# Optimization experiments

Hardware: AMD Instinct MI355X
Metric: run time of the kernel (lower is better)

The kernel has to match this reference:

```python
import jax, jax.numpy as jnp
import numpy as np

N_NODES = 100000
N_EDGES = 1600000
G_DIM, H1_DIM, H2_DIM = 128, 64, 64
N_REL = 8          # 2 * n_speakers**2, n_speakers=2
N_BASES = 30


def setup_inputs() -> dict:
    key = jax.random.key(0)
    ks = jax.random.split(key, 12)
    sc = lambda *s: 1.0 / np.sqrt(s[0])
    return {
        "node_features": jax.random.normal(ks[0], (N_NODES, G_DIM), jnp.float32),
        "edge_index": jax.random.randint(ks[1], (2, N_EDGES), 0, N_NODES),
        "edge_norm": jax.random.uniform(ks[2], (N_EDGES,), jnp.float32),
        "edge_type": jax.random.randint(ks[3], (N_EDGES,), 0, N_REL),
        # RGCNConv params (basis decomposition)
        "basis": jax.random.normal(ks[4], (N_BASES, G_DIM, H1_DIM), jnp.float32) * sc(G_DIM),
        "comp": jax.random.normal(ks[5], (N_REL, N_BASES), jnp.float32) * sc(N_BASES),
        "root": jax.random.normal(ks[6], (G_DIM, H1_DIM), jnp.float32) * sc(G_DIM),
        "bias1": jnp.zeros((H1_DIM,), jnp.float32),
        # GraphConv params
        "w_rel": jax.random.normal(ks[7], (H1_DIM, H2_DIM), jnp.float32) * sc(H1_DIM),
        "b_rel": jnp.zeros((H2_DIM,), jnp.float32),
        "w_root": jax.random.normal(ks[8], (H1_DIM, H2_DIM), jnp.float32) * sc(H1_DIM),
    }


def reference(node_features, edge_index, edge_norm, edge_type,
              basis, comp, root, bias1, w_rel, b_rel, w_root):
    N = node_features.shape[0]
    src, dst = edge_index[0], edge_index[1]

    # ---- RGCNConv: per-relation mean aggregation, basis-decomposed weights ----
    W = jnp.einsum('rb,bio->rio', comp, basis)          # [R, g, h1]
    x_src = node_features[src]                           # [E, g] gather
    out1 = node_features @ root + bias1                  # root + bias
    for r in range(N_REL):                               # fixed small relation set
        m = (edge_type == r).astype(node_features.dtype)  # [E]
        s = jax.ops.segment_sum(x_src * m[:, None], dst, num_segments=N)  # [N, g]
        cnt = jax.ops.segment_sum(m, dst, num_segments=N)                 # [N]
        h = s / jnp.maximum(cnt, 1.0)[:, None]            # mean aggr (0 if no edges)
        out1 = out1 + h @ W[r]

    # ---- GraphConv: sum of x_j * edge_weight -> lin_rel, plus lin_root ----
    agg = jax.ops.segment_sum(out1[src] * edge_norm[:, None], dst, num_segments=N)
    out2 = agg @ w_rel + b_rel + out1 @ w_root
    return out2
```

## Files before the change

### kernel.cpp

```cpp
#include <hip/hip_runtime.h>
#include <hip/hip_bf16.h>

#define NN 100000
#define NE 1600000
#define GD 128
#define H1 64
#define H2 64
#define NREL 8
#define NBASES 30
#define NBTOT 576

#define NPB 256
#define NBUCK ((NN + NPB - 1) / NPB)
#define NWGA 128
#define ECHUNK ((NE + NWGA - 1) / NWGA)

typedef __attribute__((ext_vector_type(8))) short bf16x8;
typedef __attribute__((ext_vector_type(4))) float f32x4;

static __device__ __forceinline__ unsigned short f2bf(float x) {
    __hip_bfloat16 h = __float2bfloat16(x);
    return *reinterpret_cast<unsigned short*>(&h);
}
static __device__ __forceinline__ float bf2f(unsigned short u) {
    return __uint_as_float(((unsigned)u) << 16);
}
static __device__ __forceinline__ float bflo(unsigned u) {
    return __uint_as_float(u << 16);
}
static __device__ __forceinline__ float bfhi(unsigned u) {
    return __uint_as_float(u & 0xffff0000u);
}

__global__ void prep_kernel(const float* __restrict__ basis,
                            const float* __restrict__ comp,
                            const float* __restrict__ root,
                            const float* __restrict__ w_rel,
                            const float* __restrict__ w_root,
                            unsigned short* __restrict__ WcatT,
                            unsigned short* __restrict__ B2T)
{
    int idx = blockIdx.x * blockDim.x + threadIdx.x;
    const int totalW = NBTOT * GD;
    if (idx < totalW) {
        int c = idx / GD;
        int i = idx % GD;
        float v;
        if (c < NREL * H1) {
            int r = c >> 6, o = c & 63;
            float acc = 0.f;
            #pragma unroll 5
            for (int b = 0; b < NBASES; ++b)
                acc += comp[r * NBASES + b] * basis[(b * GD + i) * H1 + o];
            v = acc;
        } else {
            v = root[i * H1 + (c - NREL * H1)];
        }
        WcatT[idx] = f2bf(v);
    } else {
        int j = idx - totalW;
        if (j < H2 * GD) {
            int o = j / GD, i = j % GD;
            float v = (i < H1) ? w_rel[i * H2 + o] : w_root[(i - H1) * H2 + o];
            B2T[j] = f2bf(v);
        }
    }
}

__global__ __launch_bounds__(512)
void bucket_count(const int* __restrict__ ei, unsigned* __restrict__ bcnt)
{
    __shared__ unsigned l[NBUCK];
    int t = threadIdx.x;
    int c0 = blockIdx.x * ECHUNK;
    int c1 = c0 + ECHUNK; if (c1 > NE) c1 = NE;
    for (int i = t; i < NBUCK; i += 512) l[i] = 0;
    __syncthreads();
    for (int e = c0 + t; e < c1; e += 512)
        atomicAdd(&l[ei[NE + e] >> 8], 1u);
    __syncthreads();
    for (int i = t; i < NBUCK; i += 512)
        if (l[i]) atomicAdd(&bcnt[i], l[i]);
}

__global__ __launch_bounds__(512)
void bucket_scan(const unsigned* __restrict__ bcnt,
                 unsigned* __restrict__ boff,
                 unsigned* __restrict__ bcur,
                 unsigned* __restrict__ off)
{
    __shared__ unsigned s[512];
    int t = threadIdx.x;
    unsigned v = (t < NBUCK) ? bcnt[t] : 0u;
    s[t] = v;
    __syncthreads();
    for (int st = 1; st < 512; st <<= 1) {
        unsigned u = (t >= st) ? s[t - st] : 0u;
        __syncthreads();
        s[t] += u;
        __syncthreads();
    }
    if (t < NBUCK) { boff[t] = s[t] - v; bcur[t] = s[t] - v; }
    if (t == 511) { boff[NBUCK] = s[511]; off[NN] = s[511]; }
}

__global__ __launch_bounds__(512)
void partition_a(const int* __restrict__ ei, const int* __restrict__ et,
                 const float* __restrict__ enorm,
                 unsigned* __restrict__ bcur,
                 uint2* __restrict__ tmp)
{
    __shared__ unsigned lcnt[NBUCK], wbase[NBUCK], lcur[NBUCK];
    int t = threadIdx.x;
    int c0 = blockIdx.x * ECHUNK;
    int c1 = c0 + ECHUNK; if (c1 > NE) c1 = NE;
    for (int i = t; i < NBUCK; i += 512) { lcnt[i] = 0; lcur[i] = 0; }
    __syncthreads();
    for (int e = c0 + t; e < c1; e += 512) {
        int dst = ei[NE + e];
        atomicAdd(&lcnt[dst >> 8], 1u);
    }
    __syncthreads();
    for (int i = t; i < NBUCK; i += 512)
        wbase[i] = atomicAdd(&bcur[i], lcnt[i]);
    __syncthreads();
    for (int e = c0 + t; e < c1; e += 512) {
        int src = ei[e], dst = ei[NE + e], r = et[e];
        int b = dst >> 8;
        unsigned pos = wbase[b] + atomicAdd(&lcur[b], 1u);
        unsigned dl = (unsigned)(dst & (NPB - 1));
        tmp[pos] = make_uint2((dl << 24) | ((unsigned)src << 3) | (unsigned)r,
                              __float_as_uint(enorm[e]));
    }
}

__global__ __launch_bounds__(512)
void partition_b(const unsigned* __restrict__ boff,
                 const uint2* __restrict__ tmp,
                 uint2* __restrict__ csr,
                 unsigned* __restrict__ off,
                 unsigned* __restrict__ cnt)
{
    __shared__ unsigned lcnt[NPB * NREL];
    __shared__ unsigned sscan[256];
    __shared__ unsigned lcur[NPB];
    int b = blockIdx.x, t = threadIdx.x;
    int nlo = b * NPB;
    int nn = NN - nlo; if (nn > NPB) nn = NPB;
    for (int i = t; i < NPB * NREL; i += 512) lcnt[i] = 0;
    __syncthreads();
    unsigned bstart = boff[b], bend = boff[b + 1];
    for (unsigned j = bstart + t; j < bend; j += 512) {
        unsigned x = tmp[j].x;
        atomicAdd(&lcnt[((x >> 24) << 3) | (x & 7u)], 1u);
    }
    __syncthreads();
    unsigned tot = 0;
    if (t < 256) {
        if (t < nn) {
            #pragma unroll
            for (int r = 0; r < NREL; ++r) tot += lcnt[t * NREL + r];
        }
        sscan[t] = tot;
    }
    __syncthreads();
    for (int st = 1; st < 256; st <<= 1) {
        unsigned u = (t < 256 && t >= st) ? sscan[t - st] : 0u;
        __syncthreads();
        if (t < 256) sscan[t] += u;
        __syncthreads();
    }
    if (t < nn) {
        unsigned ex = bstart + sscan[t] - tot;
        off[nlo + t] = ex;
        lcur[t] = ex;
        *reinterpret_cast<uint4*>(&cnt[(size_t)(nlo + t) * NREL]) =
            *reinterpret_cast<uint4*>(&lcnt[t * NREL]);
        *reinterpret_cast<uint4*>(&cnt[(size_t)(nlo + t) * NREL + 4]) =
            *reinterpret_cast<uint4*>(&lcnt[t * NREL + 4]);
    }
    __syncthreads();
    for (unsigned j = bstart + t; j < bend; j += 512) {
        uint2 rec = tmp[j];
        unsigned dl = rec.x >> 24;
        unsigned p = atomicAdd(&lcur[dl], 1u);
        csr[p] = make_uint2(rec.x & 0x00FFFFFFu, rec.y);
    }
}

template<int MODE>
__global__ __launch_bounds__(256)
void mfma_gemm(const void* __restrict__ Avoid,
               const unsigned short* __restrict__ Bt,
               int M,
               const float* __restrict__ bias,
               unsigned short* __restrict__ y,
               unsigned short* __restrict__ root1b,
               float* __restrict__ out)
{
    constexpr int NT = (MODE == 0) ? 9 : 1;
    __shared__ unsigned short Alds[128 * 128];
    __shared__ unsigned short Blds[64 * 128];

    int tid = threadIdx.x;
    int m0 = blockIdx.x * 128;
    int w = tid >> 6, l = tid & 63;
    int lr = l & 15, lk = l >> 4;

    uint4 breg0, breg1, breg2, breg3;
    {
        int c0 = (0 * 256 + tid) >> 4, s0 = tid & 15;
        int c1 = (1 * 256 + tid) >> 4;
        int c2 = (2 * 256 + tid) >> 4;
        int c3 = (3 * 256 + tid) >> 4;
        breg0 = *reinterpret_cast<const uint4*>(&Bt[(size_t)c0 * GD + s0 * 8]);
        breg1 = *reinterpret_cast<const uint4*>(&Bt[(size_t)c1 * GD + s0 * 8]);
        breg2 = *reinterpret_cast<const uint4*>(&Bt[(size_t)c2 * GD + s0 * 8]);
        breg3 = *reinterpret_cast<const uint4*>(&Bt[(size_t)c3 * GD + s0 * 8]);
    }

    if (MODE == 0) {
        const float* A = (const float*)Avoid;
        #pragma unroll
        for (int p = 0; p < 16; ++p) {
            int f = p * 256 + tid;
            int r = f >> 5;
            int c4 = f & 31;
            float4 av = make_float4(0.f, 0.f, 0.f, 0.f);
            if (m0 + r < M)
                av = *reinterpret_cast<const float4*>(&A[(size_t)(m0 + r) * GD + c4 * 4]);
            ushort4 bv;
            bv.x = f2bf(av.x); bv.y = f2bf(av.y); bv.z = f2bf(av.z); bv.w = f2bf(av.w);
            int slot = (c4 >> 1) ^ (r & 7);
            int byte = r * 256 + (slot << 4) + ((c4 & 1) << 3);
            *reinterpret_cast<ushort4*>(reinterpret_cast<char*>(Alds) + byte) = bv;
        }
    } else {
        const unsigned short* A = (const unsigned short*)Avoid;
        #pragma unroll
        for (int p = 0; p < 8; ++p) {
            int f = p * 256 + tid;
            int r = f >> 4;
            int slot = f & 15;
            uint4 v = make_uint4(0u, 0u, 0u, 0u);
            if (m0 + r < M)
                v = *reinterpret_cast<const uint4*>(&A[(size_t)(m0 + r) * GD + slot * 8]);
            int byte = r * 256 + ((slot ^ (r & 7)) << 4);
            *reinterpret_cast<uint4*>(reinterpret_cast<char*>(Alds) + byte) = v;
        }
    }

    {
        int c = (0 * 256 + tid) >> 4, s = tid & 15;
        *reinterpret_cast<uint4*>(reinterpret_cast<char*>(Blds) + c * 256 + ((s ^ (c & 7)) << 4)) = breg0;
        c = (1 * 256 + tid) >> 4;
        *reinterpret_cast<uint4*>(reinterpret_cast<char*>(Blds) + c * 256 + ((s ^ (c & 7)) << 4)) = breg1;
        c = (2 * 256 + tid) >> 4;
        *reinterpret_cast<uint4*>(reinterpret_cast<char*>(Blds) + c * 256 + ((s ^ (c & 7)) << 4)) = breg2;
        c = (3 * 256 + tid) >> 4;
        *reinterpret_cast<uint4*>(reinterpret_cast<char*>(Blds) + c * 256 + ((s ^ (c & 7)) << 4)) = breg3;
    }
    asm volatile("s_waitcnt lgkmcnt(0)" ::: "memory");
    __builtin_amdgcn_sched_barrier(0);
    __builtin_amdgcn_s_barrier();
    __builtin_amdgcn_sched_barrier(0);

    #pragma unroll 1
    for (int nt = 0; nt < NT; ++nt) {
        if (nt + 1 < NT) {
            int c = (0 * 256 + tid) >> 4, s = tid & 15;
            breg0 = *reinterpret_cast<const uint4*>(&Bt[(size_t)((nt + 1) * 64 + c) * GD + s * 8]);
            c = (1 * 256 + tid) >> 4;
            breg1 = *reinterpret_cast<const uint4*>(&Bt[(size_t)((nt + 1) * 64 + c) * GD + s * 8]);
            c = (2 * 256 + tid) >> 4;
            breg2 = *reinterpret_cast<const uint4*>(&Bt[(size_t)((nt + 1) * 64 + c) * GD + s * 8]);
            c = (3 * 256 + tid) >> 4;
            breg3 = *reinterpret_cast<const uint4*>(&Bt[(size_t)((nt + 1) * 64 + c) * GD + s * 8]);
        }

        f32x4 acc[2][4];
        #pragma unroll
        for (int i = 0; i < 2; ++i)
            #pragma unroll
            for (int j = 0; j < 4; ++j)
                acc[i][j] = (f32x4){0.f, 0.f, 0.f, 0.f};

        #pragma unroll
        for (int ks = 0; ks < 4; ++ks) {
            int q = 4 * ks + lk;
            int sA = q ^ (lr & 7);
            bf16x8 a0 = *reinterpret_cast<const bf16x8*>(
                reinterpret_cast<char*>(Alds) + (w * 32 + 0 * 16 + lr) * 256 + (sA << 4));
            bf16x8 a1 = *reinterpret_cast<const bf16x8*>(
                reinterpret_cast<char*>(Alds) + (w * 32 + 1 * 16 + lr) * 256 + (sA << 4));
            #pragma unroll
            for (int cf = 0; cf < 4; ++cf) {
                bf16x8 b = *reinterpret_cast<const bf16x8*>(
                    reinterpret_cast<char*>(Blds) + (cf * 16 + lr) * 256 + (sA << 4));
                acc[0][cf] = __builtin_amdgcn_mfma_f32_16x16x32_bf16(b, a0, acc[0][cf], 0, 0, 0);
                acc[1][cf] = __builtin_amdgcn_mfma_f32_16x16x32_bf16(b, a1, acc[1][cf], 0, 0, 0);
            }
        }

        #pragma unroll
        for (int rf = 0; rf < 2; ++rf) {
            int row = m0 + w * 32 + rf * 16 + lr;
            if (row < M) {
                #pragma unroll
                for (int cf = 0; cf < 4; ++cf) {
                    int cb = cf * 16 + lk * 4;
                    f32x4 v = acc[rf][cf];
                    if (MODE == 0) {
                        if (nt < 8) {
                            ushort4 pv;
                            pv.x = f2bf(v[0]); pv.y = f2bf(v[1]);
                            pv.z = f2bf(v[2]); pv.w = f2bf(v[3]);
                            *reinterpret_cast<ushort4*>(&y[(size_t)row * 512 + nt * 64 + cb]) = pv;
                        } else {
                            float4 bb = *reinterpret_cast<const float4*>(&bias[cb]);
                            ushort4 pv;
                            pv.x = f2bf(v[0] + bb.x); pv.y = f2bf(v[1] + bb.y);
                            pv.z = f2bf(v[2] + bb.z); pv.w = f2bf(v[3] + bb.w);
                            *reinterpret_cast<ushort4*>(&root1b[(size_t)row * 64 + cb]) = pv;
                        }
                    } else {
                        float4 bb = *reinterpret_cast<const float4*>(&bias[cb]);
                        float4 ov;
                        ov.x = v[0] + bb.x; ov.y = v[1] + bb.y;
                        ov.z = v[2] + bb.z; ov.w = v[3] + bb.w;
                        *reinterpret_cast<float4*>(&out[(size_t)row * 64 + cb]) = ov;
                    }
                }
            }
        }

        if (nt + 1 < NT) {
            asm volatile("s_waitcnt lgkmcnt(0)" ::: "memory");
            __builtin_amdgcn_sched_barrier(0);
            __builtin_amdgcn_s_barrier();
            __builtin_amdgcn_sched_barrier(0);
            int c = (0 * 256 + tid) >> 4, s = tid & 15;
            *reinterpret_cast<uint4*>(reinterpret_cast<char*>(Blds) + c * 256 + ((s ^ (c & 7)) << 4)) = breg0;
            c = (1 * 256 + tid) >> 4;
            *reinterpret_cast<uint4*>(reinterpret_cast<char*>(Blds) + c * 256 + ((s ^ (c & 7)) << 4)) = breg1;
            c = (2 * 256 + tid) >> 4;
            *reinterpret_cast<uint4*>(reinterpret_cast<char*>(Blds) + c * 256 + ((s ^ (c & 7)) << 4)) = breg2;
            c = (3 * 256 + tid) >> 4;
            *reinterpret_cast<uint4*>(reinterpret_cast<char*>(Blds) + c * 256 + ((s ^ (c & 7)) << 4)) = breg3;
            asm volatile("s_waitcnt lgkmcnt(0)" ::: "memory");
            __builtin_amdgcn_sched_barrier(0);
            __builtin_amdgcn_s_barrier();
            __builtin_amdgcn_sched_barrier(0);
        }
    }
}

__global__ void rgcn_aggregate(const unsigned* __restrict__ off,
                               const uint2* __restrict__ csr,
                               const unsigned* __restrict__ cnt,
                               const unsigned short* __restrict__ y,
                               const unsigned short* __restrict__ root1b,
                               unsigned short* __restrict__ abuf)
{
    int gid = blockIdx.x * blockDim.x + threadIdx.x;
    int n = gid >> 6;
    int l = gid & 63;
    if (n >= NN) return;
    int g = l >> 4;
    int sl = l & 15;
    unsigned myc = (l < NREL) ? cnt[(size_t)n * NREL + l] : 1u;
    float myinv = 1.0f / (float)(myc > 0u ? myc : 1u);
    unsigned s = off[n], e = off[n + 1];
    float a0 = 0.f, a1 = 0.f, a2 = 0.f, a3 = 0.f;
    float b0 = 0.f, b1 = 0.f, b2 = 0.f, b3 = 0.f;
    unsigned i = s;
    for (; i + 8 <= e; i += 8) {
        uint2 rA = csr[i + g];
        uint2 rB = csr[i + 4 + g];
        uint2 vA = *reinterpret_cast<const uint2*>(&y[(size_t)rA.x * 64 + sl * 4]);
        uint2 vB = *reinterpret_cast<const uint2*>(&y[(size_t)rB.x * 64 + sl * 4]);
        float wA = __shfl(myinv, (int)(rA.x & 7));
        float wB = __shfl(myinv, (int)(rB.x & 7));
        a0 += wA * bflo(vA.x); a1 += wA * bfhi(vA.x);
        a2 += wA * bflo(vA.y); a3 += wA * bfhi(vA.y);
        b0 += wB * bflo(vB.x); b1 += wB * bfhi(vB.x);
        b2 += wB * bflo(vB.y); b3 += wB * bfhi(vB.y);
    }
    if (i + 4 <= e) {
        uint2 rA = csr[i + g];
        uint2 vA = *reinterpret_cast<const uint2*>(&y[(size_t)rA.x * 64 + sl * 4]);
        float wA = __shfl(myinv, (int)(rA.x & 7));
        a0 += wA * bflo(vA.x); a1 += wA * bfhi(vA.x);
        a2 += wA * bflo(vA.y); a3 += wA * bfhi(vA.y);
        i += 4;
    }
    if (i < e) {
        unsigned idx = i + (unsigned)g;
        bool valid = idx < e;
        uint2 r = csr[valid ? idx : i];
        uint2 v = *reinterpret_cast<const uint2*>(&y[(size_t)r.x * 64 + sl * 4]);
        float w = __shfl(myinv, (int)(r.x & 7));
        if (!valid) w = 0.f;
        b0 += w * bflo(v.x); b1 += w * bfhi(v.x);
        b2 += w * bflo(v.y); b3 += w * bfhi(v.y);
    }
    a0 += b0; a1 += b1; a2 += b2; a3 += b3;
    a0 += __shfl_xor(a0, 16); a0 += __shfl_xor(a0, 32);
    a1 += __shfl_xor(a1, 16); a1 += __shfl_xor(a1, 32);
    a2 += __shfl_xor(a2, 16); a2 += __shfl_xor(a2, 32);
    a3 += __shfl_xor(a3, 16); a3 += __shfl_xor(a3, 32);
    if (g == 0) {
        uint2 rb = *reinterpret_cast<const uint2*>(&root1b[(size_t)n * 64 + sl * 4]);
        ushort4 pv;
        pv.x = f2bf(bflo(rb.x) + a0);
        pv.y = f2bf(bfhi(rb.x) + a1);
        pv.z = f2bf(bflo(rb.y) + a2);
        pv.w = f2bf(bfhi(rb.y) + a3);
        *reinterpret_cast<ushort4*>(&abuf[(size_t)n * 128 + 64 + sl * 4]) = pv;
    }
}

__global__ void graph_aggregate(const unsigned* __restrict__ off,
                                const uint2* __restrict__ csr,
                                unsigned short* __restrict__ abuf)
{
    int gid = blockIdx.x * blockDim.x + threadIdx.x;
    int n = gid >> 6;
    int l = gid & 63;
    if (n >= NN) return;
    int g = l >> 4;
    int sl = l & 15;
    unsigned s = off[n], e = off[n + 1];
    float a0 = 0.f, a1 = 0.f, a2 = 0.f, a3 = 0.f;
    float b0 = 0.f, b1 = 0.f, b2 = 0.f, b3 = 0.f;
    unsigned i = s;
    for (; i + 8 <= e; i += 8) {
        uint2 rA = csr[i + g];
        uint2 rB = csr[i + 4 + g];
        uint2 vA = *reinterpret_cast<const uint2*>(&abuf[(size_t)(rA.x >> 3) * 128 + 64 + sl * 4]);
        uint2 vB = *reinterpret_cast<const uint2*>(&abuf[(size_t)(rB.x >> 3) * 128 + 64 + sl * 4]);
        float wA = __uint_as_float(rA.y);
        float wB = __uint_as_float(rB.y);
        a0 += wA * bflo(vA.x); a1 += wA * bfhi(vA.x);
        a2 += wA * bflo(vA.y); a3 += wA * bfhi(vA.y);
        b0 += wB * bflo(vB.x); b1 += wB * bfhi(vB.x);
        b2 += wB * bflo(vB.y); b3 += wB * bfhi(vB.y);
    }
    if (i + 4 <= e) {
        uint2 rA = csr[i + g];
        uint2 vA = *reinterpret_cast<const uint2*>(&abuf[(size_t)(rA.x >> 3) * 128 + 64 + sl * 4]);
        float wA = __uint_as_float(rA.y);
        a0 += wA * bflo(vA.x); a1 += wA * bfhi(vA.x);
        a2 += wA * bflo(vA.y); a3 += wA * bfhi(vA.y);
        i += 4;
    }
    if (i < e) {
        unsigned idx = i + (unsigned)g;
        bool valid = idx < e;
        uint2 r = csr[valid ? idx : i];
        uint2 v = *reinterpret_cast<const uint2*>(&abuf[(size_t)(r.x >> 3) * 128 + 64 + sl * 4]);
        float w = valid ? __uint_as_float(r.y) : 0.f;
        b0 += w * bflo(v.x); b1 += w * bfhi(v.x);
        b2 += w * bflo(v.y); b3 += w * bfhi(v.y);
    }
    a0 += b0; a1 += b1; a2 += b2; a3 += b3;
    a0 += __shfl_xor(a0, 16); a0 += __shfl_xor(a0, 32);
    a1 += __shfl_xor(a1, 16); a1 += __shfl_xor(a1, 32);
    a2 += __shfl_xor(a2, 16); a2 += __shfl_xor(a2, 32);
    a3 += __shfl_xor(a3, 16); a3 += __shfl_xor(a3, 32);
    if (g == 0) {
        ushort4 pv;
        pv.x = f2bf(a0); pv.y = f2bf(a1); pv.z = f2bf(a2); pv.w = f2bf(a3);
        *reinterpret_cast<ushort4*>(&abuf[(size_t)n * 128 + sl * 4]) = pv;
    }
}

extern "C" void kernel_launch(void* const* d_in, const int* in_sizes, int n_in,
                              void* d_out, int out_size, void* d_ws, size_t ws_size,
                              hipStream_t stream)
{
    const float* node_features = (const float*)d_in[0];
    const int*   edge_index    = (const int*)d_in[1];
    const float* edge_norm     = (const float*)d_in[2];
    const int*   edge_type     = (const int*)d_in[3];
    const float* basis         = (const float*)d_in[4];
    const float* comp          = (const float*)d_in[5];
    const float* root          = (const float*)d_in[6];
    const float* bias1         = (const float*)d_in[7];
    const float* w_rel         = (const float*)d_in[8];
    const float* b_rel         = (const float*)d_in[9];
    const float* w_root        = (const float*)d_in[10];
    float* out = (float*)d_out;

    char* ws = (char*)d_ws;
    size_t o = 0;
    auto alloc = [&](size_t bytes) -> void* {
        o = (o + 511) & ~(size_t)511;
        void* p = ws + o;
        o += bytes;
        return p;
    };
    unsigned short* WcatT = (unsigned short*)alloc((size_t)NBTOT * GD * 2);
    unsigned short* B2T   = (unsigned short*)alloc((size_t)H2 * GD * 2);
    unsigned* cnt      = (unsigned*)alloc((size_t)NN * NREL * 4);
    unsigned* off_     = (unsigned*)alloc((size_t)(NN + 1) * 4);
    unsigned* bcnt     = (unsigned*)alloc((size_t)NBUCK * 4);
    unsigned* boff     = (unsigned*)alloc((size_t)(NBUCK + 1) * 4);
    unsigned* bcur     = (unsigned*)alloc((size_t)NBUCK * 4);
    uint2*    csr      = (uint2*)alloc((size_t)NE * 8);
    unsigned short* y  = (unsigned short*)alloc((size_t)NN * 512 * 2);
    unsigned short* root1b = (unsigned short*)alloc((size_t)NN * 64 * 2);
    unsigned short* abuf = (unsigned short*)alloc((size_t)NN * 128 * 2);
    uint2*    tmp      = (uint2*)abuf;

    hipMemsetAsync(bcnt, 0, (size_t)NBUCK * 4, stream);

    prep_kernel<<<(NBTOT * GD + H2 * GD + 255) / 256, 256, 0, stream>>>(
        basis, comp, root, w_rel, w_root, WcatT, B2T);

    bucket_count<<<NWGA, 512, 0, stream>>>(edge_index, bcnt);
    bucket_scan<<<1, 512, 0, stream>>>(bcnt, boff, bcur, off_);
    partition_a<<<NWGA, 512, 0, stream>>>(edge_index, edge_type, edge_norm, bcur, tmp);
    partition_b<<<NBUCK, 512, 0, stream>>>(boff, tmp, csr, off_, cnt);

    int gblk = (NN + 127) / 128;
    mfma_gemm<0><<<gblk, 256, 0, stream>>>(node_features, WcatT, NN, bias1, y, root1b, nullptr);

    rgcn_aggregate<<<(NN * 64 + 255) / 256, 256, 0, stream>>>(off_, csr, cnt, y, root1b, abuf);

    graph_aggregate<<<(NN * 64 + 255) / 256, 256, 0, stream>>>(off_, csr, abuf);

    mfma_gemm<1><<<gblk, 256, 0, stream>>>(abuf, B2T, NN, b_rel, nullptr, nullptr, out);
}
```

Measured before the change: 248.5 us.

## Split GEMM column tiles across grid Y and pre-convert features to bf16

Adds a separate kernel that converts the fp32 node features to bf16 into the abuf scratch space. The first GEMM's 9-iteration loop over 64-column tiles becomes a second grid dimension, so each block computes one tile. B fragments are loaded straight from global memory into registers, which removes the B shared-memory staging and its barriers. This gives more parallelism and shorter blocks. In exchange, each A tile is reloaded from global memory 9 times and an extra launch plus a bf16 copy of the features is added.

```diff
diff --git a/kernel.cpp b/kernel.cpp
--- a/kernel.cpp
+++ b/kernel.cpp
@@ -67,6 +67,21 @@
     }
 }
 
+__global__ __launch_bounds__(256)
+void cvt_kernel(const float* __restrict__ in, unsigned short* __restrict__ outb)
+{
+    int i = blockIdx.x * blockDim.x + threadIdx.x;
+    const int total = NN * GD / 8;
+    if (i >= total) return;
+    float4 a = *reinterpret_cast<const float4*>(&in[(size_t)i * 8]);
+    float4 b = *reinterpret_cast<const float4*>(&in[(size_t)i * 8 + 4]);
+    ushort4 p0, p1;
+    p0.x = f2bf(a.x); p0.y = f2bf(a.y); p0.z = f2bf(a.z); p0.w = f2bf(a.w);
+    p1.x = f2bf(b.x); p1.y = f2bf(b.y); p1.z = f2bf(b.z); p1.w = f2bf(b.w);
+    *reinterpret_cast<ushort4*>(&outb[(size_t)i * 8])     = p0;
+    *reinterpret_cast<ushort4*>(&outb[(size_t)i * 8 + 4]) = p1;
+}
+
 __global__ __launch_bounds__(512)
 void bucket_count(const int* __restrict__ ei, unsigned* __restrict__ bcnt)
 {
@@ -190,7 +205,7 @@
 
 template<int MODE>
 __global__ __launch_bounds__(256)
-void mfma_gemm(const void* __restrict__ Avoid,
+void mfma_gemm(const unsigned short* __restrict__ A,
                const unsigned short* __restrict__ Bt,
                int M,
                const float* __restrict__ bias,
@@ -198,159 +213,88 @@
                unsigned short* __restrict__ root1b,
                float* __restrict__ out)
 {
-    constexpr int NT = (MODE == 0) ? 9 : 1;
     __shared__ unsigned short Alds[128 * 128];
-    __shared__ unsigned short Blds[64 * 128];
 
     int tid = threadIdx.x;
     int m0 = blockIdx.x * 128;
+    int nt = blockIdx.y;
     int w = tid >> 6, l = tid & 63;
     int lr = l & 15, lk = l >> 4;
 
-    uint4 breg0, breg1, breg2, breg3;
-    {
-        int c0 = (0 * 256 + tid) >> 4, s0 = tid & 15;
-        int c1 = (1 * 256 + tid) >> 4;
-        int c2 = (2 * 256 + tid) >> 4;
-        int c3 = (3 * 256 + tid) >> 4;
-        breg0 = *reinterpret_cast<const uint4*>(&Bt[(size_t)c0 * GD + s0 * 8]);
-        breg1 = *reinterpret_cast<const uint4*>(&Bt[(size_t)c1 * GD + s0 * 8]);
-        breg2 = *reinterpret_cast<const uint4*>(&Bt[(size_t)c2 * GD + s0 * 8]);
-        breg3 = *reinterpret_cast<const uint4*>(&Bt[(size_t)c3 * GD + s0 * 8]);
-    }
-
-    if (MODE == 0) {
-        const float* A = (const float*)Avoid;
-        #pragma unroll
-        for (int p = 0; p < 16; ++p) {
-            int f = p * 256 + tid;
-            int r = f >> 5;
-            int c4 = f & 31;
-            float4 av = make_float4(0.f, 0.f, 0.f, 0.f);
-            if (m0 + r < M)
-                av = *reinterpret_cast<const float4*>(&A[(size_t)(m0 + r) * GD + c4 * 4]);
-            ushort4 bv;
-            bv.x = f2bf(av.x); bv.y = f2bf(av.y); bv.z = f2bf(av.z); bv.w = f2bf(av.w);
-            int slot = (c4 >> 1) ^ (r & 7);
-            int byte = r * 256 + (slot << 4) + ((c4 & 1) << 3);
-            *reinterpret_cast<ushort4*>(reinterpret_cast<char*>(Alds) + byte) = bv;
-        }
-    } else {
-        const unsigned short* A = (const unsigned short*)Avoid;
-        #pragma unroll
-        for (int p = 0; p < 8; ++p) {
-            int f = p * 256 + tid;
-            int r = f >> 4;
-            int slot = f & 15;
-            uint4 v = make_uint4(0u, 0u, 0u, 0u);
-            if (m0 + r < M)
-                v = *reinterpret_cast<const uint4*>(&A[(size_t)(m0 + r) * GD + slot * 8]);
-            int byte = r * 256 + ((slot ^ (r & 7)) << 4);
-            *reinterpret_cast<uint4*>(reinterpret_cast<char*>(Alds) + byte) = v;
-        }
-    }
-
-    {
-        int c = (0 * 256 + tid) >> 4, s = tid & 15;
-        *reinterpret_cast<uint4*>(reinterpret_cast<char*>(Blds) + c * 256 + ((s ^ (c & 7)) << 4)) = breg0;
-        c = (1 * 256 + tid) >> 4;
-        *reinterpret_cast<uint4*>(reinterpret_cast<char*>(Blds) + c * 256 + ((s ^ (c & 7)) << 4)) = breg1;
-        c = (2 * 256 + tid) >> 4;
-        *reinterpret_cast<uint4*>(reinterpret_cast<char*>(Blds) + c * 256 + ((s ^ (c & 7)) << 4)) = breg2;
-        c = (3 * 256 + tid) >> 4;
-        *reinterpret_cast<uint4*>(reinterpret_cast<char*>(Blds) + c * 256 + ((s ^ (c & 7)) << 4)) = breg3;
-    }
-    asm volatile("s_waitcnt lgkmcnt(0)" ::: "memory");
-    __builtin_amdgcn_sched_barrier(0);
-    __builtin_amdgcn_s_barrier();
-    __builtin_amdgcn_sched_barrier(0);
-
-    #pragma unroll 1
-    for (int nt = 0; nt < NT; ++nt) {
-        if (nt + 1 < NT) {
-            int c = (0 * 256 + tid) >> 4, s = tid & 15;
-            breg0 = *reinterpret_cast<const uint4*>(&Bt[(size_t)((nt + 1) * 64 + c) * GD + s * 8]);
-            c = (1 * 256 + tid) >> 4;
-            breg1 = *reinterpret_cast<const uint4*>(&Bt[(size_t)((nt + 1) * 64 + c) * GD + s * 8]);
-            c = (2 * 256 + tid) >> 4;
-            breg2 = *reinterpret_cast<const uint4*>(&Bt[(size_t)((nt + 1) * 64 + c) * GD + s * 8]);
-            c = (3 * 256 + tid) >> 4;
-            breg3 = *reinterpret_cast<const uint4*>(&Bt[(size_t)((nt + 1) * 64 + c) * GD + s * 8]);
-        }
-
-        f32x4 acc[2][4];
-        #pragma unroll
-        for (int i = 0; i < 2; ++i)
-            #pragma unroll
-            for (int j = 0; j < 4; ++j)
-                acc[i][j] = (f32x4){0.f, 0.f, 0.f, 0.f};
-
+    bf16x8 bfrag[4][4];
+    #pragma unroll
+    for (int cf = 0; cf < 4; ++cf)
         #pragma unroll
         for (int ks = 0; ks < 4; ++ks) {
             int q = 4 * ks + lk;
-            int sA = q ^ (lr & 7);
-            bf16x8 a0 = *reinterpret_cast<const bf16x8*>(
-                reinterpret_cast<char*>(Alds) + (w * 32 + 0 * 16 + lr) * 256 + (sA << 4));
-            bf16x8 a1 = *reinterpret_cast<const bf16x8*>(
-                reinterpret_cast<char*>(Alds) + (w * 32 + 1 * 16 + lr) * 256 + (sA << 4));
+            bfrag[cf][ks] = *reinterpret_cast<const bf16x8*>(
+                &Bt[(size_t)(nt * 64 + cf * 16 + lr) * GD + q * 8]);
+        }
+
+    #pragma unroll
+    for (int p = 0; p < 8; ++p) {
+        int f = p * 256 + tid;
+        int r = f >> 4;
+        int slot = f & 15;
+        uint4 v = make_uint4(0u, 0u, 0u, 0u);
+        if (m0 + r < M)
+            v = *reinterpret_cast<const uint4*>(&A[(size_t)(m0 + r) * GD + slot * 8]);
+        int byte = r * 256 + ((slot ^ (r & 7)) << 4);
+        *reinterpret_cast<uint4*>(reinterpret_cast<char*>(Alds) + byte) = v;
+    }
+    __syncthreads();
+
+    f32x4 acc[2][4];
+    #pragma unroll
+    for (int i = 0; i < 2; ++i)
+        #pragma unroll
+        for (int j = 0; j < 4; ++j)
+            acc[i][j] = (f32x4){0.f, 0.f, 0.f, 0.f};
+
+    #pragma unroll
+    for (int ks = 0; ks < 4; ++ks) {
+        int q = 4 * ks + lk;
+        int sA = q ^ (lr & 7);
+        bf16x8 a0 = *reinterpret_cast<const bf16x8*>(
+            reinterpret_cast<char*>(Alds) + (w * 32 + 0 * 16 + lr) * 256 + (sA << 4));
+        bf16x8 a1 = *reinterpret_cast<const bf16x8*>(
+            reinterpret_cast<char*>(Alds) + (w * 32 + 1 * 16 + lr) * 256 + (sA << 4));
+        #pragma unroll
+        for (int cf = 0; cf < 4; ++cf) {
+            acc[0][cf] = __builtin_amdgcn_mfma_f32_16x16x32_bf16(bfrag[cf][ks], a0, acc[0][cf], 0, 0, 0);
+            acc[1][cf] = __builtin_amdgcn_mfma_f32_16x16x32_bf16(bfrag[cf][ks], a1, acc[1][cf], 0, 0, 0);
+        }
+    }
+
+    #pragma unroll
+    for (int rf = 0; rf < 2; ++rf) {
+        int row = m0 + w * 32 + rf * 16 + lr;
+        if (row < M) {
             #pragma unroll
             for (int cf = 0; cf < 4; ++cf) {
-                bf16x8 b = *reinterpret_cast<const bf16x8*>(
-                    reinterpret_cast<char*>(Blds) + (cf * 16 + lr) * 256 + (sA << 4));
-                acc[0][cf] = __builtin_amdgcn_mfma_f32_16x16x32_bf16(b, a0, acc[0][cf], 0, 0, 0);
-                acc[1][cf] = __builtin_amdgcn_mfma_f32_16x16x32_bf16(b, a1, acc[1][cf], 0, 0, 0);
-            }
-        }
-
-        #pragma unroll
-        for (int rf = 0; rf < 2; ++rf) {
-            int row = m0 + w * 32 + rf * 16 + lr;
-            if (row < M) {
-                #pragma unroll
-                for (int cf = 0; cf < 4; ++cf) {
-                    int cb = cf * 16 + lk * 4;
-                    f32x4 v = acc[rf][cf];
-                    if (MODE == 0) {
-                        if (nt < 8) {
-                            ushort4 pv;
-                            pv.x = f2bf(v[0]); pv.y = f2bf(v[1]);
-                            pv.z = f2bf(v[2]); pv.w = f2bf(v[3]);
-                            *reinterpret_cast<ushort4*>(&y[(size_t)row * 512 + nt * 64 + cb]) = pv;
-                        } else {
-                            float4 bb = *reinterpret_cast<const float4*>(&bias[cb]);
-                            ushort4 pv;
-                            pv.x = f2bf(v[0] + bb.x); pv.y = f2bf(v[1] + bb.y);
-                            pv.z = f2bf(v[2] + bb.z); pv.w = f2bf(v[3] + bb.w);
-                            *reinterpret_cast<ushort4*>(&root1b[(size_t)row * 64 + cb]) = pv;
-                        }
+                int cb = cf * 16 + lk * 4;
+                f32x4 v = acc[rf][cf];
+                if (MODE == 0) {
+                    if (nt < 8) {
+                        ushort4 pv;
+                        pv.x = f2bf(v[0]); pv.y = f2bf(v[1]);
+                        pv.z = f2bf(v[2]); pv.w = f2bf(v[3]);
+                        *reinterpret_cast<ushort4*>(&y[(size_t)row * 512 + nt * 64 + cb]) = pv;
                     } else {
                         float4 bb = *reinterpret_cast<const float4*>(&bias[cb]);
-                        float4 ov;
-                        ov.x = v[0] + bb.x; ov.y = v[1] + bb.y;
-                        ov.z = v[2] + bb.z; ov.w = v[3] + bb.w;
-                        *reinterpret_cast<float4*>(&out[(size_t)row * 64 + cb]) = ov;
+                        ushort4 pv;
+                        pv.x = f2bf(v[0] + bb.x); pv.y = f2bf(v[1] + bb.y);
+                        pv.z = f2bf(v[2] + bb.z); pv.w = f2bf(v[3] + bb.w);
+                        *reinterpret_cast<ushort4*>(&root1b[(size_t)row * 64 + cb]) = pv;
                     }
+                } else {
+                    float4 bb = *reinterpret_cast<const float4*>(&bias[cb]);
+                    float4 ov;
+                    ov.x = v[0] + bb.x; ov.y = v[1] + bb.y;
+                    ov.z = v[2] + bb.z; ov.w = v[3] + bb.w;
+                    *reinterpret_cast<float4*>(&out[(size_t)row * 64 + cb]) = ov;
                 }
             }
-        }
-
-        if (nt + 1 < NT) {
-            asm volatile("s_waitcnt lgkmcnt(0)" ::: "memory");
-            __builtin_amdgcn_sched_barrier(0);
-            __builtin_amdgcn_s_barrier();
-            __builtin_amdgcn_sched_barrier(0);
-            int c = (0 * 256 + tid) >> 4, s = tid & 15;
-            *reinterpret_cast<uint4*>(reinterpret_cast<char*>(Blds) + c * 256 + ((s ^ (c & 7)) << 4)) = breg0;
-            c = (1 * 256 + tid) >> 4;
-            *reinterpret_cast<uint4*>(reinterpret_cast<char*>(Blds) + c * 256 + ((s ^ (c & 7)) << 4)) = breg1;
-            c = (2 * 256 + tid) >> 4;
-            *reinterpret_cast<uint4*>(reinterpret_cast<char*>(Blds) + c * 256 + ((s ^ (c & 7)) << 4)) = breg2;
-            c = (3 * 256 + tid) >> 4;
-            *reinterpret_cast<uint4*>(reinterpret_cast<char*>(Blds) + c * 256 + ((s ^ (c & 7)) << 4)) = breg3;
-            asm volatile("s_waitcnt lgkmcnt(0)" ::: "memory");
-            __builtin_amdgcn_sched_barrier(0);
-            __builtin_amdgcn_s_barrier();
-            __builtin_amdgcn_sched_barrier(0);
         }
     }
 }
@@ -511,7 +455,8 @@
     unsigned short* y  = (unsigned short*)alloc((size_t)NN * 512 * 2);
     unsigned short* root1b = (unsigned short*)alloc((size_t)NN * 64 * 2);
     unsigned short* abuf = (unsigned short*)alloc((size_t)NN * 128 * 2);
-    uint2*    tmp      = (uint2*)abuf;
+    uint2*          tmp = (uint2*)abuf;
+    unsigned short* xb  = (unsigned short*)abuf;
 
     hipMemsetAsync(bcnt, 0, (size_t)NBUCK * 4, stream);
 
@@ -523,12 +468,15 @@
     partition_a<<<NWGA, 512, 0, stream>>>(edge_index, edge_type, edge_norm, bcur, tmp);
     partition_b<<<NBUCK, 512, 0, stream>>>(boff, tmp, csr, off_, cnt);
 
-    int gblk = (NN + 127) / 128;
-    mfma_gemm<0><<<gblk, 256, 0, stream>>>(node_features, WcatT, NN, bias1, y, root1b, nullptr);
+    cvt_kernel<<<(NN * GD / 8 + 255) / 256, 256, 0, stream>>>(node_features, xb);
+
+    dim3 g0((NN + 127) / 128, 9);
+    mfma_gemm<0><<<g0, 256, 0, stream>>>(xb, WcatT, NN, bias1, y, root1b, nullptr);
 
     rgcn_aggregate<<<(NN * 64 + 255) / 256, 256, 0, stream>>>(off_, csr, cnt, y, root1b, abuf);
 
     graph_aggregate<<<(NN * 64 + 255) / 256, 256, 0, stream>>>(off_, csr, abuf);
 
-    mfma_gemm<1><<<gblk, 256, 0, stream>>>(abuf, B2T, NN, b_rel, nullptr, nullptr, out);
-}
+    dim3 g1((NN + 127) / 128, 1);
+    mfma_gemm<1><<<g1, 256, 0, stream>>>(abuf, B2T, NN, b_rel, nullptr, nullptr, out);
+}
```

Result: slower. 357.8 us (+44.0%).

## Use 512-thread blocks in MFMA GEMM with one 16-row fragment per wave

Applied to the files above, without the earlier changes.

Doubles the GEMM workgroup to 512 threads (8 waves), with each wave computing a single 16-row tile instead of two. The A and B staging loads are split across twice as many threads. This is meant to raise wave-level parallelism and hide load latency during the staging and epilogue phases. In exchange, B fragments are no longer reused across two A fragments per wave, so more LDS reads are issued per MFMA, and barriers now synchronize more waves.

```diff
diff --git a/kernel.cpp b/kernel.cpp
--- a/kernel.cpp
+++ b/kernel.cpp
@@ -189,7 +189,7 @@
 }
 
 template<int MODE>
-__global__ __launch_bounds__(256)
+__global__ __launch_bounds__(512)
 void mfma_gemm(const void* __restrict__ Avoid,
                const unsigned short* __restrict__ Bt,
                int M,
@@ -207,23 +207,19 @@
     int w = tid >> 6, l = tid & 63;
     int lr = l & 15, lk = l >> 4;
 
-    uint4 breg0, breg1, breg2, breg3;
+    uint4 breg0, breg1;
     {
-        int c0 = (0 * 256 + tid) >> 4, s0 = tid & 15;
-        int c1 = (1 * 256 + tid) >> 4;
-        int c2 = (2 * 256 + tid) >> 4;
-        int c3 = (3 * 256 + tid) >> 4;
+        int c0 = tid >> 4, s0 = tid & 15;
+        int c1 = 32 + (tid >> 4);
         breg0 = *reinterpret_cast<const uint4*>(&Bt[(size_t)c0 * GD + s0 * 8]);
         breg1 = *reinterpret_cast<const uint4*>(&Bt[(size_t)c1 * GD + s0 * 8]);
-        breg2 = *reinterpret_cast<const uint4*>(&Bt[(size_t)c2 * GD + s0 * 8]);
-        breg3 = *reinterpret_cast<const uint4*>(&Bt[(size_t)c3 * GD + s0 * 8]);
     }
 
     if (MODE == 0) {
         const float* A = (const float*)Avoid;
         #pragma unroll
-        for (int p = 0; p < 16; ++p) {
-            int f = p * 256 + tid;
+        for (int p = 0; p < 8; ++p) {
+            int f = p * 512 + tid;
             int r = f >> 5;
             int c4 = f & 31;
             float4 av = make_float4(0.f, 0.f, 0.f, 0.f);
@@ -238,8 +234,8 @@
     } else {
         const unsigned short* A = (const unsigned short*)Avoid;
         #pragma unroll
-        for (int p = 0; p < 8; ++p) {
-            int f = p * 256 + tid;
+        for (int p = 0; p < 4; ++p) {
+            int f = p * 512 + tid;
             int r = f >> 4;
             int slot = f & 15;
             uint4 v = make_uint4(0u, 0u, 0u, 0u);
@@ -251,14 +247,10 @@
     }
 
     {
-        int c = (0 * 256 + tid) >> 4, s = tid & 15;
+        int c = tid >> 4, s = tid & 15;
         *reinterpret_cast<uint4*>(reinterpret_cast<char*>(Blds) + c * 256 + ((s ^ (c & 7)) << 4)) = breg0;
-        c = (1 * 256 + tid) >> 4;
+        c = 32 + (tid >> 4);
         *reinterpret_cast<uint4*>(reinterpret_cast<char*>(Blds) + c * 256 + ((s ^ (c & 7)) << 4)) = breg1;
-        c = (2 * 256 + tid) >> 4;
-        *reinterpret_cast<uint4*>(reinterpret_cast<char*>(Blds) + c * 256 + ((s ^ (c & 7)) << 4)) = breg2;
-        c = (3 * 256 + tid) >> 4;
-        *reinterpret_cast<uint4*>(reinterpret_cast<char*>(Blds) + c * 256 + ((s ^ (c & 7)) << 4)) = breg3;
     }
     asm volatile("s_waitcnt lgkmcnt(0)" ::: "memory");
     __builtin_amdgcn_sched_barrier(0);
@@ -268,68 +260,56 @@
     #pragma unroll 1
     for (int nt = 0; nt < NT; ++nt) {
         if (nt + 1 < NT) {
-            int c = (0 * 256 + tid) >> 4, s = tid & 15;
+            int c = tid >> 4, s = tid & 15;
             breg0 = *reinterpret_cast<const uint4*>(&Bt[(size_t)((nt + 1) * 64 + c) * GD + s * 8]);
-            c = (1 * 256 + tid) >> 4;
+            c = 32 + (tid >> 4);
             breg1 = *reinterpret_cast<const uint4*>(&Bt[(size_t)((nt + 1) * 64 + c) * GD + s * 8]);
-            c = (2 * 256 + tid) >> 4;
-            breg2 = *reinterpret_cast<const uint4*>(&Bt[(size_t)((nt + 1) * 64 + c) * GD + s * 8]);
-            c = (3 * 256 + tid) >> 4;
-            breg3 = *reinterpret_cast<const uint4*>(&Bt[(size_t)((nt + 1) * 64 + c) * GD + s * 8]);
-        }
-
-        f32x4 acc[2][4];
+        }
+
+        f32x4 acc[4];
         #pragma unroll
-        for (int i = 0; i < 2; ++i)
-            #pragma unroll
-            for (int j = 0; j < 4; ++j)
-                acc[i][j] = (f32x4){0.f, 0.f, 0.f, 0.f};
+        for (int j = 0; j < 4; ++j)
+            acc[j] = (f32x4){0.f, 0.f, 0.f, 0.f};
 
         #pragma unroll
         for (int ks = 0; ks < 4; ++ks) {
             int q = 4 * ks + lk;
             int sA = q ^ (lr & 7);
             bf16x8 a0 = *reinterpret_cast<const bf16x8*>(
-                reinterpret_cast<char*>(Alds) + (w * 32 + 0 * 16 + lr) * 256 + (sA << 4));
-            bf16x8 a1 = *reinterpret_cast<const bf16x8*>(
-                reinterpret_cast<char*>(Alds) + (w * 32 + 1 * 16 + lr) * 256 + (sA << 4));
+                reinterpret_cast<char*>(Alds) + (w * 16 + lr) * 256 + (sA << 4));
             #pragma unroll
             for (int cf = 0; cf < 4; ++cf) {
                 bf16x8 b = *reinterpret_cast<const bf16x8*>(
                     reinterpret_cast<char*>(Blds) + (cf * 16 + lr) * 256 + (sA << 4));
-                acc[0][cf] = __builtin_amdgcn_mfma_f32_16x16x32_bf16(b, a0, acc[0][cf], 0, 0, 0);
-                acc[1][cf] = __builtin_amdgcn_mfma_f32_16x16x32_bf16(b, a1, acc[1][cf], 0, 0, 0);
+                acc[cf] = __builtin_amdgcn_mfma_f32_16x16x32_bf16(b, a0, acc[cf], 0, 0, 0);
             }
         }
 
-        #pragma unroll
-        for (int rf = 0; rf < 2; ++rf) {
-            int row = m0 + w * 32 + rf * 16 + lr;
-            if (row < M) {
-                #pragma unroll
-                for (int cf = 0; cf < 4; ++cf) {
-                    int cb = cf * 16 + lk * 4;
-                    f32x4 v = acc[rf][cf];
-                    if (MODE == 0) {
-                        if (nt < 8) {
-                            ushort4 pv;
-                            pv.x = f2bf(v[0]); pv.y = f2bf(v[1]);
-                            pv.z = f2bf(v[2]); pv.w = f2bf(v[3]);
-                            *reinterpret_cast<ushort4*>(&y[(size_t)row * 512 + nt * 64 + cb]) = pv;
-                        } else {
-                            float4 bb = *reinterpret_cast<const float4*>(&bias[cb]);
-                            ushort4 pv;
-                            pv.x = f2bf(v[0] + bb.x); pv.y = f2bf(v[1] + bb.y);
-                            pv.z = f2bf(v[2] + bb.z); pv.w = f2bf(v[3] + bb.w);
-                            *reinterpret_cast<ushort4*>(&root1b[(size_t)row * 64 + cb]) = pv;
-                        }
+        int row = m0 + w * 16 + lr;
+        if (row < M) {
+            #pragma unroll
+            for (int cf = 0; cf < 4; ++cf) {
+                int cb = cf * 16 + lk * 4;
+                f32x4 v = acc[cf];
+                if (MODE == 0) {
+                    if (nt < 8) {
+                        ushort4 pv;
+                        pv.x = f2bf(v[0]); pv.y = f2bf(v[1]);
+                        pv.z = f2bf(v[2]); pv.w = f2bf(v[3]);
+                        *reinterpret_cast<ushort4*>(&y[(size_t)row * 512 + nt * 64 + cb]) = pv;
                     } else {
                         float4 bb = *reinterpret_cast<const float4*>(&bias[cb]);
-                        float4 ov;
-                        ov.x = v[0] + bb.x; ov.y = v[1] + bb.y;
-                        ov.z = v[2] + bb.z; ov.w = v[3] + bb.w;
-                        *reinterpret_cast<float4*>(&out[(size_t)row * 64 + cb]) = ov;
+                        ushort4 pv;
+                        pv.x = f2bf(v[0] + bb.x); pv.y = f2bf(v[1] + bb.y);
+                        pv.z = f2bf(v[2] + bb.z); pv.w = f2bf(v[3] + bb.w);
+                        *reinterpret_cast<ushort4*>(&root1b[(size_t)row * 64 + cb]) = pv;
                     }
+                } else {
+                    float4 bb = *reinterpret_cast<const float4*>(&bias[cb]);
+                    float4 ov;
+                    ov.x = v[0] + bb.x; ov.y = v[1] + bb.y;
+                    ov.z = v[2] + bb.z; ov.w = v[3] + bb.w;
+                    *reinterpret_cast<float4*>(&out[(size_t)row * 64 + cb]) = ov;
                 }
             }
         }
@@ -339,14 +319,10 @@
             __builtin_amdgcn_sched_barrier(0);
             __builtin_amdgcn_s_barrier();
             __builtin_amdgcn_sched_barrier(0);
-            int c = (0 * 256 + tid) >> 4, s = tid & 15;
+            int c = tid >> 4, s = tid & 15;
             *reinterpret_cast<uint4*>(reinterpret_cast<char*>(Blds) + c * 256 + ((s ^ (c & 7)) << 4)) = breg0;
-            c = (1 * 256 + tid) >> 4;
+            c = 32 + (tid >> 4);
             *reinterpret_cast<uint4*>(reinterpret_cast<char*>(Blds) + c * 256 + ((s ^ (c & 7)) << 4)) = breg1;
-            c = (2 * 256 + tid) >> 4;
-            *reinterpret_cast<uint4*>(reinterpret_cast<char*>(Blds) + c * 256 + ((s ^ (c & 7)) << 4)) = breg2;
-            c = (3 * 256 + tid) >> 4;
-            *reinterpret_cast<uint4*>(reinterpret_cast<char*>(Blds) + c * 256 + ((s ^ (c & 7)) << 4)) = breg3;
             asm volatile("s_waitcnt lgkmcnt(0)" ::: "memory");
             __builtin_amdgcn_sched_barrier(0);
             __builtin_amdgcn_s_barrier();
@@ -524,11 +500,11 @@
     partition_b<<<NBUCK, 512, 0, stream>>>(boff, tmp, csr, off_, cnt);
 
     int gblk = (NN + 127) / 128;
-    mfma_gemm<0><<<gblk, 256, 0, stream>>>(node_features, WcatT, NN, bias1, y, root1b, nullptr);
+    mfma_gemm<0><<<gblk, 512, 0, stream>>>(node_features, WcatT, NN, bias1, y, root1b, nullptr);
 
     rgcn_aggregate<<<(NN * 64 + 255) / 256, 256, 0, stream>>>(off_, csr, cnt, y, root1b, abuf);
 
     graph_aggregate<<<(NN * 64 + 255) / 256, 256, 0, stream>>>(off_, csr, abuf);
 
-    mfma_gemm<1><<<gblk, 256, 0, stream>>>(abuf, B2T, NN, b_rel, nullptr, nullptr, out);
-}
+    mfma_gemm<1><<<gblk, 512, 0, stream>>>(abuf, B2T, NN, b_rel, nullptr, nullptr, out);
+}
```

After: 254.4 us. +2.4%, slower.
